# Performance work log

Hardware: AMD Instinct MI355X
Metric: run time of the kernel (lower is better)

The kernel has to match this reference:

```python
import jax, jax.numpy as jnp
import numpy as np

N_HEAD = 16
N_KV_HEAD = 4
N_EMBD = 2048

def rotate_half(x):
    x1, x2 = jnp.split(x, 2, axis=-1)
    return jnp.concatenate([-x2, x1], axis=-1)

def rope_tables(T, k):
    # angles = 10000^(-2*i/k) for i in [0, k/2); cos/sin repeated twice along last dim
    inv = jnp.power(10000.0, -2.0 * jnp.arange(k // 2, dtype=jnp.float32) / k)
    ang = jnp.arange(T, dtype=jnp.float32)[:, None] * inv[None, :]  # [T, k/2]
    cos = jnp.tile(jnp.cos(ang), (1, 2))  # [T, k]
    sin = jnp.tile(jnp.sin(ang), (1, 2))
    return cos, sin

def setup_inputs() -> dict:
    key = jax.random.key(0)
    ks = jax.random.split(key, 5)
    B, T, D = 4, 1024, N_EMBD
    g, h = N_KV_HEAD, N_HEAD
    k = D // h
    s = 0.02
    return {
        'x': jax.random.normal(ks[0], (B, T, D), dtype=jnp.float32),
        'Wq': jax.random.normal(ks[1], (D, D), dtype=jnp.float32) * s,
        'Wk': jax.random.normal(ks[2], (D, g * k), dtype=jnp.float32) * s,
        'Wv': jax.random.normal(ks[3], (D, g * k), dtype=jnp.float32) * s,
        'Wo': jax.random.normal(ks[4], (D, D), dtype=jnp.float32) * s,
    }

def reference(x, Wq, Wk, Wv, Wo):
    B, T, D = x.shape
    h, g = N_HEAD, N_KV_HEAD
    k = D // h
    Q = (x @ Wq).reshape(B, T, h, k).transpose(0, 2, 1, 3)  # [B,h,T,k]
    K = (x @ Wk).reshape(B, T, g, k).transpose(0, 2, 1, 3)  # [B,g,T,k]
    V = (x @ Wv).reshape(B, T, g, k).transpose(0, 2, 1, 3)
    # GQA: repeat_interleave kv heads to match query heads
    K = jnp.repeat(K, h // g, axis=1)  # [B,h,T,k]
    V = jnp.repeat(V, h // g, axis=1)
    cos, sin = rope_tables(T, k)
    cos = cos[None, None]  # [1,1,T,k]
    sin = sin[None, None]
    Q = Q * cos + rotate_half(Q) * sin
    K = K * cos + rotate_half(K) * sin
    scores = jnp.einsum('bhqk,bhsk->bhqs', Q, K) / jnp.sqrt(jnp.float32(k))
    causal = jnp.tril(jnp.ones((T, T), dtype=bool))
    scores = jnp.where(causal[None, None], scores, -jnp.inf)
    A = jax.nn.softmax(scores, axis=-1)
    Y = jnp.einsum('bhqs,bhsk->bhqk', A, V)
    Y = Y.transpose(0, 2, 1, 3).reshape(B, T, D)
    return Y @ Wo
```

## Files before the change

kernel.cpp:

```cpp
#include <hip/hip_runtime.h>
#include <math.h>

#define B_ 4
#define T_ 1024
#define D_ 2048
#define NH 16
#define NKV 4
#define HD 128
#define KV_D 512
#define QKV_S 2560

typedef __attribute__((ext_vector_type(8))) short short8;
typedef __attribute__((ext_vector_type(4))) float f32x4;

__device__ __forceinline__ ushort f2b(float f) {
    unsigned u = __float_as_uint(f);
    return (ushort)((u + 0x7fffu + ((u >> 16) & 1u)) >> 16);
}
__device__ __forceinline__ float b2f(ushort u) {
    return __uint_as_float((unsigned)u << 16);
}

#if __has_builtin(__builtin_amdgcn_exp2f)
#define EXP2F(x) __builtin_amdgcn_exp2f(x)
#else
#define EXP2F(x) __expf((x) * 0.6931471805599453f)
#endif

#define ASYNC_COPY16(g, l)                                                  \
    __builtin_amdgcn_global_load_lds(                                       \
        (const __attribute__((address_space(1))) void*)(g),                 \
        (__attribute__((address_space(3))) void*)(l), 16, 0, 0)

#define MFMA16(ap, bp, cc) cc = __builtin_amdgcn_mfma_f32_16x16x32_bf16(ap, bp, cc, 0, 0, 0)

__global__ __launch_bounds__(256) void prep_all(const float* __restrict__ x,
                                                const float* __restrict__ Wq,
                                                const float* __restrict__ Wk,
                                                const float* __restrict__ Wv,
                                                const float* __restrict__ Wo,
                                                ushort* __restrict__ xb,
                                                ushort* __restrict__ WqkvT,
                                                ushort* __restrict__ WoT,
                                                float2* __restrict__ tab) {
    __shared__ float tile[64][65];
    const int bid = blockIdx.x;
    const int tid = threadIdx.x;
    if (bid < 8192) {
        const int i = bid * 256 + tid;
        const float4 v = ((const float4*)x)[i];
        ushort4 u;
        u.x = f2b(v.x); u.y = f2b(v.y); u.z = f2b(v.z); u.w = f2b(v.w);
        ((ushort4*)xb)[i] = u;
        return;
    }
    if (bid >= 10752) {
        const int idx = (bid - 10752) * 256 + tid;
        const int t = idx >> 6, i = idx & 63;
        const float inv = exp2f((float)i * (-13.287712379549449f / 64.0f));
        const float ang = (float)t * inv;
        tab[idx] = make_float2(cosf(ang), sinf(ang));
        return;
    }
    const float* W;
    ushort* WT;
    int N, rb;
    if (bid < 9216)      { W = Wq; WT = WqkvT;                           N = D_;   rb = bid - 8192; }
    else if (bid < 9472) { W = Wk; WT = WqkvT + (size_t)D_ * D_;         N = KV_D; rb = bid - 9216; }
    else if (bid < 9728) { W = Wv; WT = WqkvT + (size_t)(D_+KV_D) * D_;  N = KV_D; rb = bid - 9472; }
    else                 { W = Wo; WT = WoT;                             N = D_;   rb = bid - 9728; }
    const int bxn = N / 64;
    const int n0 = (rb % bxn) * 64, k0 = (rb / bxn) * 64;
    const int tx = tid & 15, ty = tid >> 4;
#pragma unroll
    for (int i = 0; i < 4; ++i) {
        const int r = ty + i * 16;
        const float4 v = *(const float4*)&W[(size_t)(k0 + r) * N + n0 + tx * 4];
        tile[r][tx * 4 + 0] = v.x;
        tile[r][tx * 4 + 1] = v.y;
        tile[r][tx * 4 + 2] = v.z;
        tile[r][tx * 4 + 3] = v.w;
    }
    __syncthreads();
    const int n = tid >> 2, ch = (tid & 3) * 16;
    ushort tmp[16];
#pragma unroll
    for (int j = 0; j < 16; ++j) tmp[j] = f2b(tile[ch + j][n]);
    ushort* orow = WT + (size_t)(n0 + n) * D_ + k0 + ch;
    *(short8*)&orow[0] = *(short8*)&tmp[0];
    *(short8*)&orow[8] = *(short8*)&tmp[8];
}

__global__ __launch_bounds__(256) void gemm_qkv(const ushort* __restrict__ A,
                                                const ushort* __restrict__ BT,
                                                ushort* __restrict__ QKV,
                                                ushort* __restrict__ Vt,
                                                const float2* __restrict__ tab) {
    __shared__ ushort smem[128 * 136];
    ushort* As = smem;
    ushort* Bs = smem + 4096;
    const int K = D_;
    const int tid = threadIdx.x;
    const int m0 = blockIdx.y * 128, n0 = blockIdx.x * 128;
    const int hid = n0 >> 7;
    const int wave = tid >> 6, lane = tid & 63;
    const int wm = (wave >> 1) * 64, wn = (wave & 1) * 64;
    const int lrow = lane & 15;
    const int quad = lane >> 4;

    f32x4 acc[4][4];
    const f32x4 zero = {0.f, 0.f, 0.f, 0.f};
#pragma unroll
    for (int i = 0; i < 4; ++i)
#pragma unroll
        for (int j = 0; j < 4; ++j) acc[i][j] = zero;

    const int srow = tid >> 2;
    const int scol = (tid & 3) * 8;
    const ushort* Ag = A + (size_t)(m0 + srow) * K + scol;
    const ushort* Bg = BT + (size_t)(n0 + srow) * K + scol;
    ushort* AsT = As + tid * 8;
    ushort* BsT = Bs + tid * 8;

    for (int k0 = 0; k0 < K; k0 += 32) {
        ASYNC_COPY16(Ag + k0, AsT);
        ASYNC_COPY16(Ag + k0 + (size_t)64 * K, AsT + 64 * 32);
        ASYNC_COPY16(Bg + k0, BsT);
        ASYNC_COPY16(Bg + k0 + (size_t)64 * K, BsT + 64 * 32);
        __syncthreads();

        short8 a[4], b[4];
#pragma unroll
        for (int mt = 0; mt < 4; ++mt)
            a[mt] = *(const short8*)&As[(wm + mt * 16 + lrow) * 32 + quad * 8];
#pragma unroll
        for (int nt = 0; nt < 4; ++nt)
            b[nt] = *(const short8*)&Bs[(wn + nt * 16 + lrow) * 32 + quad * 8];
#pragma unroll
        for (int mt = 0; mt < 4; ++mt)
#pragma unroll
            for (int nt = 0; nt < 4; ++nt)
                acc[mt][nt] = __builtin_amdgcn_mfma_f32_16x16x32_bf16(
                    a[mt], b[nt], acc[mt][nt], 0, 0, 0);
        __syncthreads();
    }

    ushort* Epi = smem;
#pragma unroll
    for (int mt = 0; mt < 4; ++mt)
#pragma unroll
        for (int nt = 0; nt < 4; ++nt)
#pragma unroll
            for (int r = 0; r < 4; ++r)
                Epi[(wm + mt * 16 + quad * 4 + r) * 136 + wn + nt * 16 + lrow] =
                    f2b(acc[mt][nt][r]);
    __syncthreads();

    const int b = m0 >> 10;
    const int t0 = m0 & 1023;

    if (hid < NH + NKV) {
        const bool isQ = hid < NH;
        const size_t colbase = isQ ? hid * HD : (size_t)D_ + (hid - NH) * HD;
        const float sc = isQ ? (0.08838834764831845f * 1.4426950408889634f) : 1.0f;
        const int r = tid >> 1;
        const int hf = tid & 1;
        const int t = t0 + r;
        ushort* orow = QKV + (size_t)(m0 + r) * QKV_S + colbase;
        const float4* tab4 = (const float4*)tab;
#pragma unroll
        for (int jj = 0; jj < 4; ++jj) {
            const int dbase = hf * 32 + jj * 8;
            const short8 lo = *(const short8*)&Epi[r * 136 + dbase];
            const short8 hi = *(const short8*)&Epi[r * 136 + 64 + dbase];
            ushort olo[8], ohi[8];
#pragma unroll
            for (int k = 0; k < 4; ++k) {
                const float4 cs = tab4[((t * 64 + dbase) >> 1) + k];
                const float x1a = b2f(lo[2 * k]),     x2a = b2f(hi[2 * k]);
                const float x1b = b2f(lo[2 * k + 1]), x2b = b2f(hi[2 * k + 1]);
                olo[2 * k]     = f2b((x1a * cs.x - x2a * cs.y) * sc);
                ohi[2 * k]     = f2b((x2a * cs.x + x1a * cs.y) * sc);
                olo[2 * k + 1] = f2b((x1b * cs.z - x2b * cs.w) * sc);
                ohi[2 * k + 1] = f2b((x2b * cs.z + x1b * cs.w) * sc);
            }
            *(short8*)&orow[dbase]      = *(short8*)olo;
            *(short8*)&orow[dbase + 64] = *(short8*)ohi;
        }
    } else {
        const int kv = hid - (NH + NKV);
        const int d = tid & 127;
        const int hf = tid >> 7;
        ushort* vrow = Vt + ((size_t)((b * NKV + kv) * HD + d)) * T_ + t0 + hf * 64;
#pragma unroll
        for (int jj = 0; jj < 8; ++jj) {
            ushort pk[8];
#pragma unroll
            for (int k = 0; k < 8; ++k)
                pk[k] = Epi[(hf * 64 + jj * 8 + k) * 136 + d];
            *(short8*)&vrow[jj * 8] = *(short8*)pk;
        }
    }
}

__global__ __launch_bounds__(256) void gemm_bf16(const ushort* __restrict__ A,
                                                 const ushort* __restrict__ BT,
                                                 float* __restrict__ C,
                                                 int M, int N, int K) {
    __shared__ ushort As[128 * 64];
    __shared__ ushort Bs[128 * 64];
    const int tid = threadIdx.x;
    const int m0 = blockIdx.y * 128, n0 = blockIdx.x * 128;
    const int wave = tid >> 6, lane = tid & 63;
    const int wm = (wave >> 1) * 64, wn = (wave & 1) * 64;
    const int lrow = lane & 15;
    const int quad = lane >> 4;

    f32x4 acc[4][4];
    const f32x4 zero = {0.f, 0.f, 0.f, 0.f};
#pragma unroll
    for (int i = 0; i < 4; ++i)
#pragma unroll
        for (int j = 0; j < 4; ++j) acc[i][j] = zero;

    const int srow = tid >> 3;
    const int scol = ((tid & 7) * 8) ^ ((srow & 7) << 3);
    const ushort* Ag = A + (size_t)(m0 + srow) * K + scol;
    const ushort* Bg = BT + (size_t)(n0 + srow) * K + scol;
    ushort* AsT = As + tid * 8;
    ushort* BsT = Bs + tid * 8;
    const int swr = (lrow & 7) << 3;

    for (int k0 = 0; k0 < K; k0 += 64) {
#pragma unroll
        for (int c = 0; c < 4; ++c) {
            ASYNC_COPY16(Ag + k0 + (size_t)(c * 32) * K, AsT + c * 2048);
            ASYNC_COPY16(Bg + k0 + (size_t)(c * 32) * K, BsT + c * 2048);
        }
        __syncthreads();

#pragma unroll
        for (int ks = 0; ks < 2; ++ks) {
            const int col = (quad * 8) ^ (ks * 32) ^ swr;
            short8 a[4], b[4];
#pragma unroll
            for (int mt = 0; mt < 4; ++mt)
                a[mt] = *(const short8*)&As[(wm + mt * 16 + lrow) * 64 + col];
#pragma unroll
            for (int nt = 0; nt < 4; ++nt)
                b[nt] = *(const short8*)&Bs[(wn + nt * 16 + lrow) * 64 + col];
#pragma unroll
            for (int mt = 0; mt < 4; ++mt)
#pragma unroll
                for (int nt = 0; nt < 4; ++nt)
                    MFMA16(a[mt], b[nt], acc[mt][nt]);
        }
        __syncthreads();
    }

    const int crow = quad * 4;
    const int ccol = lrow;
#pragma unroll
    for (int mt = 0; mt < 4; ++mt)
#pragma unroll
        for (int nt = 0; nt < 4; ++nt)
#pragma unroll
            for (int r = 0; r < 4; ++r)
                C[(size_t)(m0 + wm + mt * 16 + crow + r) * N +
                  n0 + wn + nt * 16 + ccol] = acc[mt][nt][r];
}

__global__ __launch_bounds__(256) void attn_mfma(const ushort* __restrict__ QKV,
                                                 const ushort* __restrict__ Vt,
                                                 ushort* __restrict__ Yb) {
    __shared__ ushort Ks[64][136];
    __shared__ ushort Vs[128][72];
    __shared__ ushort Ps[4][16][72];

    const int bh = blockIdx.x;
    const int qt = (int)gridDim.y - 1 - (int)blockIdx.y;
    const int b = bh >> 4, h = bh & 15;
    const int kvh = h >> 2;
    const int q0 = qt * 64;
    const int tid = threadIdx.x;
    const int wave = tid >> 6, lane = tid & 63;
    const int ln = lane & 15, quad = lane >> 4;

    short8 qf[4];
    {
        const ushort* qp = QKV + ((size_t)(b * T_ + q0 + wave * 16 + ln)) * QKV_S + h * HD + quad * 8;
#pragma unroll
        for (int f = 0; f < 4; ++f) qf[f] = *(const short8*)(qp + f * 32);
    }

    const size_t kv_row = (size_t)((b * NKV + kvh) * HD);
    const ushort* const Vbase = Vt + kv_row * T_;
    const ushort* const Kbase = QKV + ((size_t)(b * T_)) * QKV_S + D_ + kvh * HD;

    short8 kreg[4], vreg[4];
#define LOAD_KV(s0_)                                                        \
    do {                                                                    \
        _Pragma("unroll")                                                   \
        for (int c = 0; c < 4; ++c) {                                       \
            const int cid = tid + 256 * c;                                  \
            const int s = cid >> 4, ch = cid & 15;                          \
            kreg[c] = *(const short8*)&Kbase[((size_t)((s0_) + s)) * QKV_S + ch * 8]; \
        }                                                                   \
        _Pragma("unroll")                                                   \
        for (int c = 0; c < 4; ++c) {                                       \
            const int cid = tid + 256 * c;                                  \
            const int d = cid >> 3, ch = cid & 7;                           \
            vreg[c] = *(const short8*)&Vbase[(size_t)d * T_ + (s0_) + ch * 8]; \
        }                                                                   \
    } while (0)

    f32x4 acc[8];
    const f32x4 zero = {0.f, 0.f, 0.f, 0.f};
#pragma unroll
    for (int j = 0; j < 8; ++j) acc[j] = zero;
    float m_r[4], l_r[4];
#pragma unroll
    for (int r = 0; r < 4; ++r) { m_r[r] = -INFINITY; l_r[r] = 0.f; }

    const int qrow = q0 + wave * 16 + quad * 4;

    LOAD_KV(0);

    for (int kt = 0; kt <= qt; ++kt) {
        const int s0 = kt * 64;
        __syncthreads();
#pragma unroll
        for (int c = 0; c < 4; ++c) {
            const int cid = tid + 256 * c;
            const int s = cid >> 4, ch = cid & 15;
            *(short8*)&Ks[s][ch * 8] = kreg[c];
        }
#pragma unroll
        for (int c = 0; c < 4; ++c) {
            const int cid = tid + 256 * c;
            const int d = cid >> 3, ch = cid & 7;
            *(short8*)&Vs[d][ch * 8] = vreg[c];
        }
        __syncthreads();

        if (kt < qt) LOAD_KV(s0 + 64);

        float sc[4][4];
#pragma unroll
        for (int ct = 0; ct < 4; ++ct) {
            f32x4 s4 = zero;
#pragma unroll
            for (int f = 0; f < 4; ++f)
                s4 = __builtin_amdgcn_mfma_f32_16x16x32_bf16(
                    qf[f], *(const short8*)&Ks[ct * 16 + ln][f * 32 + quad * 8], s4, 0, 0, 0);
#pragma unroll
            for (int r = 0; r < 4; ++r) sc[ct][r] = s4[r];
        }
        if (kt == qt) {
#pragma unroll
            for (int ct = 0; ct < 4; ++ct)
#pragma unroll
                for (int r = 0; r < 4; ++r)
                    if (s0 + ct * 16 + ln > qrow + r) sc[ct][r] = -INFINITY;
        }
        float alpha[4];
#pragma unroll
        for (int r = 0; r < 4; ++r) {
            float mx = fmaxf(fmaxf(sc[0][r], sc[1][r]), fmaxf(sc[2][r], sc[3][r]));
            mx = fmaxf(mx, __shfl_xor(mx, 1));
            mx = fmaxf(mx, __shfl_xor(mx, 2));
            mx = fmaxf(mx, __shfl_xor(mx, 4));
            mx = fmaxf(mx, __shfl_xor(mx, 8));
            const float mnew = fmaxf(m_r[r], mx);
            alpha[r] = EXP2F(m_r[r] - mnew);
            m_r[r] = mnew;
#pragma unroll
            for (int ct = 0; ct < 4; ++ct) sc[ct][r] = EXP2F(sc[ct][r] - mnew);
            float sum = (sc[0][r] + sc[1][r]) + (sc[2][r] + sc[3][r]);
            sum += __shfl_xor(sum, 1);
            sum += __shfl_xor(sum, 2);
            sum += __shfl_xor(sum, 4);
            sum += __shfl_xor(sum, 8);
            l_r[r] = l_r[r] * alpha[r] + sum;
        }
#pragma unroll
        for (int ct = 0; ct < 4; ++ct)
#pragma unroll
            for (int r = 0; r < 4; ++r)
                Ps[wave][quad * 4 + r][ct * 16 + ln] = f2b(sc[ct][r]);
#pragma unroll
        for (int j = 0; j < 8; ++j)
#pragma unroll
            for (int r = 0; r < 4; ++r) acc[j][r] *= alpha[r];
        const short8 pa0 = *(const short8*)&Ps[wave][ln][quad * 8];
        const short8 pa1 = *(const short8*)&Ps[wave][ln][32 + quad * 8];
#pragma unroll
        for (int j = 0; j < 8; ++j) {
            acc[j] = __builtin_amdgcn_mfma_f32_16x16x32_bf16(
                pa0, *(const short8*)&Vs[j * 16 + ln][quad * 8], acc[j], 0, 0, 0);
            acc[j] = __builtin_amdgcn_mfma_f32_16x16x32_bf16(
                pa1, *(const short8*)&Vs[j * 16 + ln][32 + quad * 8], acc[j], 0, 0, 0);
        }
    }
#undef LOAD_KV

    float invl[4];
#pragma unroll
    for (int r = 0; r < 4; ++r) invl[r] = 1.f / l_r[r];
    ushort* yb = Yb + ((size_t)(b * T_ + qrow)) * D_ + h * HD + ln;
#pragma unroll
    for (int r = 0; r < 4; ++r)
#pragma unroll
        for (int j = 0; j < 8; ++j)
            yb[(size_t)r * D_ + j * 16] = f2b(acc[j][r] * invl[r]);
}

extern "C" void kernel_launch(void* const* d_in, const int* in_sizes, int n_in,
                              void* d_out, int out_size, void* d_ws, size_t ws_size,
                              hipStream_t stream) {
    const float* x  = (const float*)d_in[0];
    const float* Wq = (const float*)d_in[1];
    const float* Wk = (const float*)d_in[2];
    const float* Wv = (const float*)d_in[3];
    const float* Wo = (const float*)d_in[4];
    float* out = (float*)d_out;

    char* w = (char*)d_ws;
    ushort* xb    = (ushort*)w;  w += (size_t)4096 * D_ * 2;
    ushort* WqkvT = (ushort*)w;  w += (size_t)3072 * D_ * 2;
    ushort* QKV   = (ushort*)w;  w += (size_t)4096 * QKV_S * 2;
    ushort* Vt    = (ushort*)w;  w += (size_t)B_ * KV_D * T_ * 2;
    ushort* Yb    = (ushort*)w;  w += (size_t)4096 * D_ * 2;
    ushort* WoT   = (ushort*)w;  w += (size_t)D_ * D_ * 2;
    float2* tab   = (float2*)w;  w += (size_t)T_ * 64 * 8;

    const int M = B_ * T_;
    dim3 blk(256);

    prep_all<<<11008, blk, 0, stream>>>(x, Wq, Wk, Wv, Wo, xb, WqkvT, WoT, tab);

    gemm_qkv<<<dim3(3072 / 128, M / 128), blk, 0, stream>>>(xb, WqkvT, QKV, Vt, tab);

    attn_mfma<<<dim3(B_ * NH, T_ / 64), blk, 0, stream>>>(QKV, Vt, Yb);

    gemm_bf16<<<dim3(D_ / 128, M / 128), blk, 0, stream>>>(Yb, WoT, out, M, D_, D_);
}
```

Before: 278.6 us.

## Process two 64-row query groups per attention block to reuse K/V tiles

Each attention block now handles 128 query rows, as two 64-row groups, instead of 64. Every K/V tile staged in shared memory serves both groups, which halves K/V global loads and LDS staging per query row. The grid shrinks to 512 blocks, and s_setprio raises wave priority around the MFMA sections. In exchange, register pressure roughly doubles for accumulators and Q fragments (launch bounds now request 3 blocks), and there are fewer blocks to balance the causal workload.

```diff
diff --git a/kernel.cpp b/kernel.cpp
--- a/kernel.cpp
+++ b/kernel.cpp
@@ -270,9 +270,9 @@
                   n0 + wn + nt * 16 + ccol] = acc[mt][nt][r];
 }
 
-__global__ __launch_bounds__(256) void attn_mfma(const ushort* __restrict__ QKV,
-                                                 const ushort* __restrict__ Vt,
-                                                 ushort* __restrict__ Yb) {
+__global__ __launch_bounds__(256, 3) void attn_mfma(const ushort* __restrict__ QKV,
+                                                    const ushort* __restrict__ Vt,
+                                                    ushort* __restrict__ Yb) {
     __shared__ ushort Ks[64][136];
     __shared__ ushort Vs[128][72];
     __shared__ ushort Ps[4][16][72];
@@ -281,20 +281,20 @@
     const int qt = (int)gridDim.y - 1 - (int)blockIdx.y;
     const int b = bh >> 4, h = bh & 15;
     const int kvh = h >> 2;
-    const int q0 = qt * 64;
+    const int q0 = qt * 128;
     const int tid = threadIdx.x;
     const int wave = tid >> 6, lane = tid & 63;
     const int ln = lane & 15, quad = lane >> 4;
 
-    short8 qf[4];
-    {
-        const ushort* qp = QKV + ((size_t)(b * T_ + q0 + wave * 16 + ln)) * QKV_S + h * HD + quad * 8;
-#pragma unroll
-        for (int f = 0; f < 4; ++f) qf[f] = *(const short8*)(qp + f * 32);
-    }
-
-    const size_t kv_row = (size_t)((b * NKV + kvh) * HD);
-    const ushort* const Vbase = Vt + kv_row * T_;
+    short8 qf[2][4];
+#pragma unroll
+    for (int g = 0; g < 2; ++g) {
+        const ushort* qp = QKV + ((size_t)(b * T_ + q0 + g * 64 + wave * 16 + ln)) * QKV_S + h * HD + quad * 8;
+#pragma unroll
+        for (int f = 0; f < 4; ++f) qf[g][f] = *(const short8*)(qp + f * 32);
+    }
+
+    const ushort* const Vbase = Vt + ((size_t)((b * NKV + kvh) * HD)) * T_;
     const ushort* const Kbase = QKV + ((size_t)(b * T_)) * QKV_S + D_ + kvh * HD;
 
     short8 kreg[4], vreg[4];
@@ -314,19 +314,23 @@
         }                                                                   \
     } while (0)
 
-    f32x4 acc[8];
+    f32x4 acc[2][8];
     const f32x4 zero = {0.f, 0.f, 0.f, 0.f};
 #pragma unroll
-    for (int j = 0; j < 8; ++j) acc[j] = zero;
-    float m_r[4], l_r[4];
-#pragma unroll
-    for (int r = 0; r < 4; ++r) { m_r[r] = -INFINITY; l_r[r] = 0.f; }
-
-    const int qrow = q0 + wave * 16 + quad * 4;
+    for (int g = 0; g < 2; ++g)
+#pragma unroll
+        for (int j = 0; j < 8; ++j) acc[g][j] = zero;
+    float m_r[2][4], l_r[2][4];
+#pragma unroll
+    for (int g = 0; g < 2; ++g)
+#pragma unroll
+        for (int r = 0; r < 4; ++r) { m_r[g][r] = -INFINITY; l_r[g][r] = 0.f; }
+
+    const int ktmax = 2 * qt + 1;
 
     LOAD_KV(0);
 
-    for (int kt = 0; kt <= qt; ++kt) {
+    for (int kt = 0; kt <= ktmax; ++kt) {
         const int s0 = kt * 64;
         __syncthreads();
 #pragma unroll
@@ -343,76 +347,90 @@
         }
         __syncthreads();
 
-        if (kt < qt) LOAD_KV(s0 + 64);
-
-        float sc[4][4];
-#pragma unroll
-        for (int ct = 0; ct < 4; ++ct) {
-            f32x4 s4 = zero;
-#pragma unroll
-            for (int f = 0; f < 4; ++f)
-                s4 = __builtin_amdgcn_mfma_f32_16x16x32_bf16(
-                    qf[f], *(const short8*)&Ks[ct * 16 + ln][f * 32 + quad * 8], s4, 0, 0, 0);
-#pragma unroll
-            for (int r = 0; r < 4; ++r) sc[ct][r] = s4[r];
-        }
-        if (kt == qt) {
+        if (kt < ktmax) LOAD_KV(s0 + 64);
+
+#pragma unroll
+        for (int g = 0; g < 2; ++g) {
+            if (kt > 2 * qt + g) continue;
+            const int qrow = q0 + g * 64 + wave * 16 + quad * 4;
+
+            float sc[4][4];
+            __builtin_amdgcn_s_setprio(1);
+#pragma unroll
+            for (int ct = 0; ct < 4; ++ct) {
+                f32x4 s4 = zero;
+#pragma unroll
+                for (int f = 0; f < 4; ++f)
+                    s4 = __builtin_amdgcn_mfma_f32_16x16x32_bf16(
+                        qf[g][f], *(const short8*)&Ks[ct * 16 + ln][f * 32 + quad * 8], s4, 0, 0, 0);
+#pragma unroll
+                for (int r = 0; r < 4; ++r) sc[ct][r] = s4[r];
+            }
+            __builtin_amdgcn_s_setprio(0);
+            if (kt == 2 * qt + g) {
+#pragma unroll
+                for (int ct = 0; ct < 4; ++ct)
+#pragma unroll
+                    for (int r = 0; r < 4; ++r)
+                        if (s0 + ct * 16 + ln > qrow + r) sc[ct][r] = -INFINITY;
+            }
+            float alpha[4];
+#pragma unroll
+            for (int r = 0; r < 4; ++r) {
+                float mx = fmaxf(fmaxf(sc[0][r], sc[1][r]), fmaxf(sc[2][r], sc[3][r]));
+                mx = fmaxf(mx, __shfl_xor(mx, 1));
+                mx = fmaxf(mx, __shfl_xor(mx, 2));
+                mx = fmaxf(mx, __shfl_xor(mx, 4));
+                mx = fmaxf(mx, __shfl_xor(mx, 8));
+                const float mnew = fmaxf(m_r[g][r], mx);
+                alpha[r] = EXP2F(m_r[g][r] - mnew);
+                m_r[g][r] = mnew;
+#pragma unroll
+                for (int ct = 0; ct < 4; ++ct) sc[ct][r] = EXP2F(sc[ct][r] - mnew);
+                float sum = (sc[0][r] + sc[1][r]) + (sc[2][r] + sc[3][r]);
+                sum += __shfl_xor(sum, 1);
+                sum += __shfl_xor(sum, 2);
+                sum += __shfl_xor(sum, 4);
+                sum += __shfl_xor(sum, 8);
+                l_r[g][r] = l_r[g][r] * alpha[r] + sum;
+            }
 #pragma unroll
             for (int ct = 0; ct < 4; ++ct)
 #pragma unroll
                 for (int r = 0; r < 4; ++r)
-                    if (s0 + ct * 16 + ln > qrow + r) sc[ct][r] = -INFINITY;
-        }
-        float alpha[4];
-#pragma unroll
-        for (int r = 0; r < 4; ++r) {
-            float mx = fmaxf(fmaxf(sc[0][r], sc[1][r]), fmaxf(sc[2][r], sc[3][r]));
-            mx = fmaxf(mx, __shfl_xor(mx, 1));
-            mx = fmaxf(mx, __shfl_xor(mx, 2));
-            mx = fmaxf(mx, __shfl_xor(mx, 4));
-            mx = fmaxf(mx, __shfl_xor(mx, 8));
-            const float mnew = fmaxf(m_r[r], mx);
-            alpha[r] = EXP2F(m_r[r] - mnew);
-            m_r[r] = mnew;
-#pragma unroll
-            for (int ct = 0; ct < 4; ++ct) sc[ct][r] = EXP2F(sc[ct][r] - mnew);
-            float sum = (sc[0][r] + sc[1][r]) + (sc[2][r] + sc[3][r]);
-            sum += __shfl_xor(sum, 1);
-            sum += __shfl_xor(sum, 2);
-            sum += __shfl_xor(sum, 4);
-            sum += __shfl_xor(sum, 8);
-            l_r[r] = l_r[r] * alpha[r] + sum;
-        }
-#pragma unroll
-        for (int ct = 0; ct < 4; ++ct)
-#pragma unroll
-            for (int r = 0; r < 4; ++r)
-                Ps[wave][quad * 4 + r][ct * 16 + ln] = f2b(sc[ct][r]);
-#pragma unroll
-        for (int j = 0; j < 8; ++j)
-#pragma unroll
-            for (int r = 0; r < 4; ++r) acc[j][r] *= alpha[r];
-        const short8 pa0 = *(const short8*)&Ps[wave][ln][quad * 8];
-        const short8 pa1 = *(const short8*)&Ps[wave][ln][32 + quad * 8];
-#pragma unroll
-        for (int j = 0; j < 8; ++j) {
-            acc[j] = __builtin_amdgcn_mfma_f32_16x16x32_bf16(
-                pa0, *(const short8*)&Vs[j * 16 + ln][quad * 8], acc[j], 0, 0, 0);
-            acc[j] = __builtin_amdgcn_mfma_f32_16x16x32_bf16(
-                pa1, *(const short8*)&Vs[j * 16 + ln][32 + quad * 8], acc[j], 0, 0, 0);
+                    Ps[wave][quad * 4 + r][ct * 16 + ln] = f2b(sc[ct][r]);
+#pragma unroll
+            for (int j = 0; j < 8; ++j)
+#pragma unroll
+                for (int r = 0; r < 4; ++r) acc[g][j][r] *= alpha[r];
+            const short8 pa0 = *(const short8*)&Ps[wave][ln][quad * 8];
+            const short8 pa1 = *(const short8*)&Ps[wave][ln][32 + quad * 8];
+            __builtin_amdgcn_s_setprio(1);
+#pragma unroll
+            for (int j = 0; j < 8; ++j) {
+                acc[g][j] = __builtin_amdgcn_mfma_f32_16x16x32_bf16(
+                    pa0, *(const short8*)&Vs[j * 16 + ln][quad * 8], acc[g][j], 0, 0, 0);
+                acc[g][j] = __builtin_amdgcn_mfma_f32_16x16x32_bf16(
+                    pa1, *(const short8*)&Vs[j * 16 + ln][32 + quad * 8], acc[g][j], 0, 0, 0);
+            }
+            __builtin_amdgcn_s_setprio(0);
         }
     }
 #undef LOAD_KV
 
-    float invl[4];
-#pragma unroll
-    for (int r = 0; r < 4; ++r) invl[r] = 1.f / l_r[r];
-    ushort* yb = Yb + ((size_t)(b * T_ + qrow)) * D_ + h * HD + ln;
-#pragma unroll
-    for (int r = 0; r < 4; ++r)
-#pragma unroll
-        for (int j = 0; j < 8; ++j)
-            yb[(size_t)r * D_ + j * 16] = f2b(acc[j][r] * invl[r]);
+#pragma unroll
+    for (int g = 0; g < 2; ++g) {
+        float invl[4];
+#pragma unroll
+        for (int r = 0; r < 4; ++r) invl[r] = 1.f / l_r[g][r];
+        const int qrow = q0 + g * 64 + wave * 16 + quad * 4;
+        ushort* yb = Yb + ((size_t)(b * T_ + qrow)) * D_ + h * HD + ln;
+#pragma unroll
+        for (int r = 0; r < 4; ++r)
+#pragma unroll
+            for (int j = 0; j < 8; ++j)
+                yb[(size_t)r * D_ + j * 16] = f2b(acc[g][j][r] * invl[r]);
+    }
 }
 
 extern "C" void kernel_launch(void* const* d_in, const int* in_sizes, int n_in,
@@ -441,7 +459,7 @@
 
     gemm_qkv<<<dim3(3072 / 128, M / 128), blk, 0, stream>>>(xb, WqkvT, QKV, Vt, tab);
 
-    attn_mfma<<<dim3(B_ * NH, T_ / 64), blk, 0, stream>>>(QKV, Vt, Yb);
+    attn_mfma<<<dim3(B_ * NH, T_ / 128), blk, 0, stream>>>(QKV, Vt, Yb);
 
     gemm_bf16<<<dim3(D_ / 128, M / 128), blk, 0, stream>>>(Yb, WoT, out, M, D_, D_);
 }
```

Measured after the change: 357.8 us. 1.28x slower.
